# Optimization experiments

Measured on AMD Instinct MI355X. Metric: run time of the kernel, lower is better.

The kernel has to match this reference:

```python
import jax, jax.numpy as jnp
import numpy as np

N_NODES = 100000
N_EDGES = 1600000
IN_DIM, HID_DIM, OUT_DIM = 256, 128, 128


def gcn_norm(edge_index, edge_weight, num_nodes):
    # Add self-loops with weight 1 (PyG GCNConv default fill_value=1.0)
    loop = jnp.arange(num_nodes, dtype=edge_index.dtype)
    src = jnp.concatenate([edge_index[0], loop])
    dst = jnp.concatenate([edge_index[1], loop])
    w = jnp.concatenate([edge_weight, jnp.ones((num_nodes,), edge_weight.dtype)])
    # Symmetric normalization: deg computed at destination over edge weights
    deg = jax.ops.segment_sum(w, dst, num_segments=num_nodes)
    dinv = jnp.where(deg > 0, jax.lax.rsqrt(deg), 0.0)
    norm = dinv[src] * w * dinv[dst]  # [E + N]
    return src, dst, norm


def gcn_conv(x, W, b, src, dst, norm, num_nodes):
    h = x @ W                                  # [N, out]
    msg = h[src] * norm[:, None]               # gather + scale, [E+N, out]
    out = jax.ops.segment_sum(msg, dst, num_segments=num_nodes)  # scatter-add
    return out + b


def setup_inputs() -> dict:
    key = jax.random.key(0)
    ks = jax.random.split(key, 8)
    x = jax.random.normal(ks[0], (N_NODES, IN_DIM), dtype=jnp.float32)
    edge_index = jax.random.randint(ks[1], (2, N_EDGES), 0, N_NODES, dtype=jnp.int64)
    edge_weight = jax.random.uniform(ks[2], (N_EDGES,), dtype=jnp.float32)
    s1 = 1.0 / np.sqrt(IN_DIM)
    s2 = 1.0 / np.sqrt(HID_DIM)
    W1 = jax.random.uniform(ks[3], (IN_DIM, HID_DIM), jnp.float32, -s1, s1)
    b1 = jnp.zeros((HID_DIM,), jnp.float32)
    W2 = jax.random.uniform(ks[4], (HID_DIM, OUT_DIM), jnp.float32, -s2, s2)
    b2 = jnp.zeros((OUT_DIM,), jnp.float32)
    return {"x": x, "edge_index": edge_index, "edge_weight": edge_weight,
            "W1": W1, "b1": b1, "W2": W2, "b2": b2}


def reference(x, edge_index, edge_weight, W1, b1, W2, b2):
    n = x.shape[0]
    src, dst, norm = gcn_norm(edge_index, edge_weight, n)
    h = jax.nn.relu(gcn_conv(x, W1, b1, src, dst, norm, n))
    out = gcn_conv(h, W2, b2, src, dst, norm, n)
    return out
```

## Files before the change

kernel.cpp:

```cpp
#include <hip/hip_runtime.h>
#include <stdint.h>

#define N_NODES 100000
#define N_EDGES 1600000
#define IN_DIM 256
#define HID_DIM 128
#define OUT_DIM 128

#define NBUCK 391
#define CHUNK 4096

typedef __attribute__((ext_vector_type(8))) short short8;
typedef __attribute__((ext_vector_type(4))) float floatx4;

__device__ __forceinline__ float bf2f(unsigned short u) {
    union { unsigned int i; float f; } v; v.i = ((unsigned int)u) << 16; return v.f;
}
__device__ __forceinline__ unsigned short f2bf(float f) {
    union { float fl; unsigned int i; } v; v.fl = f;
    unsigned int x = v.i;
    return (unsigned short)((x + 0x7fffu + ((x >> 16) & 1u)) >> 16);
}
__device__ __forceinline__ float bflo(unsigned int u) {
    union { unsigned int i; float f; } v; v.i = u << 16; return v.f;
}
__device__ __forceinline__ float bfhi(unsigned int u) {
    union { unsigned int i; float f; } v; v.i = u & 0xffff0000u; return v.f;
}
__device__ __forceinline__ float asf(unsigned int u) {
    union { unsigned int i; float f; } v; v.i = u; return v.f;
}
__device__ __forceinline__ unsigned int asu(float f) {
    union { float fl; unsigned int i; } v; v.fl = f; return v.i;
}
__device__ __forceinline__ unsigned int pack2(float a, float b) {
    unsigned int ua = asu(a), ub = asu(b);
    ua += 0x7fffu + ((ua >> 16) & 1u);
    ub += 0x7fffu + ((ub >> 16) & 1u);
    return (ua >> 16) | (ub & 0xffff0000u);
}
__device__ __forceinline__ short8 pack8(float4 a, float4 b) {
    union { unsigned int u[4]; short8 s; } r;
    r.u[0] = pack2(a.x, a.y);
    r.u[1] = pack2(a.z, a.w);
    r.u[2] = pack2(b.x, b.y);
    r.u[3] = pack2(b.z, b.w);
    return r.s;
}

__global__ void k_detect(const unsigned int* __restrict__ xu, const unsigned int* __restrict__ eu,
                         int* __restrict__ flags, int* __restrict__ bucket_cnt) {
    __shared__ int s_huge, s_odd;
    if (threadIdx.x == 0) { s_huge = 0; s_odd = 0; }
    if (threadIdx.x < NBUCK) bucket_cnt[threadIdx.x] = 0;
    __syncthreads();
    int huge = 0, odd = 0;
    for (int i = threadIdx.x; i < 1024; i += 512) {
        unsigned int b = xu[i];
        unsigned int e = (b >> 23) & 0xffu;
        if (e >= 0xf0u) huge = 1;
        if (eu[2 * i + 1] != 0) odd = 1;
    }
    if (huge) atomicOr(&s_huge, 1);
    if (odd) atomicOr(&s_odd, 1);
    __syncthreads();
    if (threadIdx.x == 0) { flags[0] = s_huge ? 0 : 1; flags[1] = s_odd ? 0 : 1; }
}

__device__ __forceinline__ int load_idx(const void* base, long long i, int i64m) {
    int v = i64m ? (int)((const long long*)base)[i] : ((const int*)base)[i];
    return v < 0 ? 0 : (v >= N_NODES ? N_NODES - 1 : v);
}
__device__ __forceinline__ float load_f(const void* base, long long i, int f32m) {
    return f32m ? ((const float*)base)[i] : bf2f(((const unsigned short*)base)[i]);
}

__global__ void k_bhist(const void* __restrict__ ei, const int* __restrict__ flags,
                        int* __restrict__ bucket_cnt, int e) {
    __shared__ int h[NBUCK];
    for (int t = threadIdx.x; t < NBUCK; t += 256) h[t] = 0;
    __syncthreads();
    int i64m = flags[1];
    int base = blockIdx.x * CHUNK;
    int end = base + CHUNK < e ? base + CHUNK : e;
    for (int i = base + threadIdx.x; i < end; i += 256) {
        int d = load_idx(ei, (long long)N_EDGES + i, i64m);
        atomicAdd(&h[d >> 8], 1);
    }
    __syncthreads();
    for (int t = threadIdx.x; t < NBUCK; t += 256)
        if (h[t]) atomicAdd(&bucket_cnt[t], h[t]);
}

__global__ void k_bscan(const int* __restrict__ bucket_cnt, int* __restrict__ bucket_base,
                        int* __restrict__ bucket_cursor, int* __restrict__ rowptr) {
    __shared__ int lds[512];
    int t = threadIdx.x;
    int v = (t < NBUCK) ? bucket_cnt[t] : 0;
    lds[t] = v;
    __syncthreads();
    for (int off = 1; off < 512; off <<= 1) {
        int x = (t >= off) ? lds[t - off] : 0;
        __syncthreads();
        lds[t] += x;
        __syncthreads();
    }
    int excl = lds[t] - v;
    if (t < NBUCK) { bucket_base[t] = excl; bucket_cursor[t] = excl; }
    if (t == 0) { bucket_base[NBUCK] = lds[NBUCK - 1]; rowptr[N_NODES] = N_EDGES; }
}

__global__ void k_bscatter(const void* __restrict__ ei, const void* __restrict__ ew,
                           const int* __restrict__ flags, int* __restrict__ bucket_cursor,
                           uint2* __restrict__ ebuf, int e) {
    __shared__ int h[NBUCK];
    for (int t = threadIdx.x; t < NBUCK; t += 256) h[t] = 0;
    __syncthreads();
    int f32m = flags[0], i64m = flags[1];
    int base = blockIdx.x * CHUNK;
    int end = base + CHUNK < e ? base + CHUNK : e;
    for (int i = base + threadIdx.x; i < end; i += 256) {
        int d = load_idx(ei, (long long)N_EDGES + i, i64m);
        atomicAdd(&h[d >> 8], 1);
    }
    __syncthreads();
    for (int t = threadIdx.x; t < NBUCK; t += 256) {
        int c = h[t];
        h[t] = c ? atomicAdd(&bucket_cursor[t], c) : 0;
    }
    __syncthreads();
    for (int i = base + threadIdx.x; i < end; i += 256) {
        int s = load_idx(ei, i, i64m);
        int d = load_idx(ei, (long long)N_EDGES + i, i64m);
        float w = load_f(ew, i, f32m);
        int b = d >> 8;
        int p = atomicAdd(&h[b], 1);
        uint2 c; c.x = (unsigned int)s | ((unsigned int)(d & 255) << 17); c.y = asu(w);
        ebuf[p] = c;
    }
}

__global__ void k_fine(const uint2* __restrict__ ebuf, const int* __restrict__ bucket_base,
                       uint2* __restrict__ csr, int* __restrict__ rowptr,
                       float* __restrict__ dinv, int n) {
    __shared__ int h[256];
    __shared__ float fw[256];
    __shared__ int c2[256];
    int t = threadIdx.x, b = blockIdx.x;
    int e0 = bucket_base[b], e1 = bucket_base[b + 1];
    h[t] = 0; fw[t] = 0.f;
    __syncthreads();
    for (int i = e0 + t; i < e1; i += 256) {
        uint2 c = ebuf[i];
        int dl = (c.x >> 17) & 255;
        atomicAdd(&h[dl], 1);
        atomicAdd(&fw[dl], asf(c.y));
    }
    __syncthreads();
    int own = h[t];
    for (int off = 1; off < 256; off <<= 1) {
        int x = (t >= off) ? h[t - off] : 0;
        __syncthreads();
        h[t] += x;
        __syncthreads();
    }
    int excl = h[t] - own;
    int node = (b << 8) + t;
    if (node < n) {
        rowptr[node] = e0 + excl;
        dinv[node] = rsqrtf(1.0f + fw[t]);
    }
    c2[t] = e0 + excl;
    __syncthreads();
    for (int i = e0 + t; i < e1; i += 256) {
        uint2 c = ebuf[i];
        int dl = (c.x >> 17) & 255;
        int p = atomicAdd(&c2[dl], 1);
        csr[p] = c;
    }
}

__global__ void k_transpose(const void* __restrict__ W1, const void* __restrict__ W2,
                            const int* __restrict__ flags,
                            unsigned short* __restrict__ W1T, unsigned short* __restrict__ W2T) {
    int i = blockIdx.x * 256 + threadIdx.x;
    int f32m = flags[0];
    if (i < IN_DIM * HID_DIM) {
        int k = i / HID_DIM, n = i % HID_DIM;
        W1T[n * IN_DIM + k] = f2bf(load_f(W1, i, f32m));
    } else {
        int j = i - IN_DIM * HID_DIM;
        if (j < HID_DIM * OUT_DIM) {
            int k = j / OUT_DIM, n = j % OUT_DIM;
            W2T[n * HID_DIM + k] = f2bf(load_f(W2, j, f32m));
        }
    }
}

template <int K, bool F32M>
__device__ __forceinline__ void gemm_loop(const void* __restrict__ A,
                                          const unsigned short* __restrict__ Bs,
                                          size_t aoff0, size_t aoff1,
                                          int quad, int l16, floatx4 (&acc)[2][8]) {
    constexpr int NCH = K / 32;
    constexpr int BMASK = K / 8 - 1;
    float4 fraw[2][2];
    short8 braw[2];
    if (F32M) {
        const float* ap = (const float*)A;
        fraw[0][0] = *(const float4*)(ap + aoff0);
        fraw[0][1] = *(const float4*)(ap + aoff0 + 4);
        fraw[1][0] = *(const float4*)(ap + aoff1);
        fraw[1][1] = *(const float4*)(ap + aoff1 + 4);
    } else {
        const unsigned short* ap = (const unsigned short*)A;
        braw[0] = *(const short8*)(ap + aoff0);
        braw[1] = *(const short8*)(ap + aoff1);
    }
#pragma unroll
    for (int ch = 0; ch < NCH; ch++) {
        float4 nf[2][2];
        short8 nb[2];
        if (ch + 1 < NCH) {
            int o = (ch + 1) * 32;
            if (F32M) {
                const float* ap = (const float*)A;
                nf[0][0] = *(const float4*)(ap + aoff0 + o);
                nf[0][1] = *(const float4*)(ap + aoff0 + o + 4);
                nf[1][0] = *(const float4*)(ap + aoff1 + o);
                nf[1][1] = *(const float4*)(ap + aoff1 + o + 4);
            } else {
                const unsigned short* ap = (const unsigned short*)A;
                nb[0] = *(const short8*)(ap + aoff0 + o);
                nb[1] = *(const short8*)(ap + aoff1 + o);
            }
        }
        short8 a0, a1;
        if (F32M) {
            a0 = pack8(fraw[0][0], fraw[0][1]);
            a1 = pack8(fraw[1][0], fraw[1][1]);
        } else {
            a0 = braw[0];
            a1 = braw[1];
        }
#pragma unroll
        for (int c = 0; c < 8; c++) {
            int col = c * 16 + l16;
            int boff = col * K + 8 * ((ch * 4 + quad + (col & 7)) & BMASK);
            short8 bf = *(const short8*)(Bs + boff);
            acc[0][c] = __builtin_amdgcn_mfma_f32_16x16x32_bf16(a0, bf, acc[0][c], 0, 0, 0);
            acc[1][c] = __builtin_amdgcn_mfma_f32_16x16x32_bf16(a1, bf, acc[1][c], 0, 0, 0);
        }
        if (ch + 1 < NCH) {
            if (F32M) {
                fraw[0][0] = nf[0][0]; fraw[0][1] = nf[0][1];
                fraw[1][0] = nf[1][0]; fraw[1][1] = nf[1][1];
            } else {
                braw[0] = nb[0]; braw[1] = nb[1];
            }
        }
    }
}

template <int K, bool RAWA>
__global__ void k_gemm(const void* __restrict__ A, const unsigned short* __restrict__ WT,
                       unsigned short* __restrict__ H, const int* __restrict__ flags, int n) {
    __shared__ unsigned short Bs[128 * K];
    for (int base = threadIdx.x * 8; base < 128 * K; base += 256 * 8) {
        int col = base / K;
        int k = base - col * K;
        int ks = (k + (col & 7) * 8) & (K - 1);
        *(short8*)(&Bs[col * K + ks]) = *(const short8*)(WT + base);
    }
    __syncthreads();

    int wave = threadIdx.x >> 6;
    int lane = threadIdx.x & 63;
    int quad = lane >> 4;
    int l16 = lane & 15;
    int rowbase = blockIdx.x * 128 + wave * 32;
    int r0 = rowbase + l16;        if (r0 >= n) r0 = n - 1;
    int r1 = rowbase + 16 + l16;   if (r1 >= n) r1 = n - 1;
    size_t aoff0 = (size_t)r0 * K + quad * 8;
    size_t aoff1 = (size_t)r1 * K + quad * 8;

    floatx4 acc[2][8];
#pragma unroll
    for (int t = 0; t < 2; t++)
#pragma unroll
        for (int c = 0; c < 8; c++) acc[t][c] = (floatx4){0.f, 0.f, 0.f, 0.f};

    int f32m = RAWA ? flags[0] : 0;
    if (RAWA && f32m)
        gemm_loop<K, true>(A, Bs, aoff0, aoff1, quad, l16, acc);
    else
        gemm_loop<K, false>(A, Bs, aoff0, aoff1, quad, l16, acc);

#pragma unroll
    for (int t = 0; t < 2; t++)
#pragma unroll
        for (int c = 0; c < 8; c++)
#pragma unroll
            for (int r = 0; r < 4; r++) {
                int grow = rowbase + t * 16 + quad * 4 + r;
                if (grow < n) H[(size_t)grow * 128 + c * 16 + l16] = f2bf(acc[t][c][r]);
            }
}

template <bool RELU, bool FINAL>
__global__ void k_aggregate(const unsigned short* __restrict__ H, const int* __restrict__ rowptr,
                            const uint2* __restrict__ csr, const float* __restrict__ dinv,
                            const void* __restrict__ bias, void* __restrict__ out,
                            const int* __restrict__ flags, int n) {
    int node = blockIdx.x * 16 + (threadIdx.x >> 4);
    int lane = threadIdx.x & 15;
    if (node >= n) return;
    int col = lane * 8;
    int f32m = flags[0];

    float a0 = 0.f, a1 = 0.f, a2 = 0.f, a3 = 0.f;
    float a4 = 0.f, a5 = 0.f, a6 = 0.f, a7 = 0.f;
    int e0 = rowptr[node], e1 = rowptr[node + 1];
    int e = e0;
    for (; e + 4 <= e1; e += 4) {
        uint2 c0 = csr[e], c1 = csr[e + 1], c2 = csr[e + 2], c3 = csr[e + 3];
        int s0 = c0.x & 0x1FFFF, s1 = c1.x & 0x1FFFF, s2 = c2.x & 0x1FFFF, s3 = c3.x & 0x1FFFF;
        uint4 h0 = *(const uint4*)(H + (size_t)s0 * 128 + col);
        uint4 h1 = *(const uint4*)(H + (size_t)s1 * 128 + col);
        uint4 h2 = *(const uint4*)(H + (size_t)s2 * 128 + col);
        uint4 h3 = *(const uint4*)(H + (size_t)s3 * 128 + col);
        float w0 = asf(c0.y) * dinv[s0], w1 = asf(c1.y) * dinv[s1];
        float w2 = asf(c2.y) * dinv[s2], w3 = asf(c3.y) * dinv[s3];
        a0 += w0 * bflo(h0.x); a1 += w0 * bfhi(h0.x); a2 += w0 * bflo(h0.y); a3 += w0 * bfhi(h0.y);
        a4 += w0 * bflo(h0.z); a5 += w0 * bfhi(h0.z); a6 += w0 * bflo(h0.w); a7 += w0 * bfhi(h0.w);
        a0 += w1 * bflo(h1.x); a1 += w1 * bfhi(h1.x); a2 += w1 * bflo(h1.y); a3 += w1 * bfhi(h1.y);
        a4 += w1 * bflo(h1.z); a5 += w1 * bfhi(h1.z); a6 += w1 * bflo(h1.w); a7 += w1 * bfhi(h1.w);
        a0 += w2 * bflo(h2.x); a1 += w2 * bfhi(h2.x); a2 += w2 * bflo(h2.y); a3 += w2 * bfhi(h2.y);
        a4 += w2 * bflo(h2.z); a5 += w2 * bfhi(h2.z); a6 += w2 * bflo(h2.w); a7 += w2 * bfhi(h2.w);
        a0 += w3 * bflo(h3.x); a1 += w3 * bfhi(h3.x); a2 += w3 * bflo(h3.y); a3 += w3 * bfhi(h3.y);
        a4 += w3 * bflo(h3.z); a5 += w3 * bfhi(h3.z); a6 += w3 * bflo(h3.w); a7 += w3 * bfhi(h3.w);
    }
    for (; e < e1; e++) {
        uint2 c0 = csr[e];
        int s0 = c0.x & 0x1FFFF;
        uint4 h0 = *(const uint4*)(H + (size_t)s0 * 128 + col);
        float w0 = asf(c0.y) * dinv[s0];
        a0 += w0 * bflo(h0.x); a1 += w0 * bfhi(h0.x); a2 += w0 * bflo(h0.y); a3 += w0 * bfhi(h0.y);
        a4 += w0 * bflo(h0.z); a5 += w0 * bfhi(h0.z); a6 += w0 * bflo(h0.w); a7 += w0 * bfhi(h0.w);
    }

    float dn = dinv[node];
    float coef = dn * dn;
    uint4 u = *(const uint4*)(H + (size_t)node * 128 + col);
    a0 = dn * a0 + coef * bflo(u.x) + load_f(bias, col, f32m);
    a1 = dn * a1 + coef * bfhi(u.x) + load_f(bias, col + 1, f32m);
    a2 = dn * a2 + coef * bflo(u.y) + load_f(bias, col + 2, f32m);
    a3 = dn * a3 + coef * bfhi(u.y) + load_f(bias, col + 3, f32m);
    a4 = dn * a4 + coef * bflo(u.z) + load_f(bias, col + 4, f32m);
    a5 = dn * a5 + coef * bfhi(u.z) + load_f(bias, col + 5, f32m);
    a6 = dn * a6 + coef * bflo(u.w) + load_f(bias, col + 6, f32m);
    a7 = dn * a7 + coef * bfhi(u.w) + load_f(bias, col + 7, f32m);

    if (RELU) {
        a0 = fmaxf(a0, 0.f); a1 = fmaxf(a1, 0.f); a2 = fmaxf(a2, 0.f); a3 = fmaxf(a3, 0.f);
        a4 = fmaxf(a4, 0.f); a5 = fmaxf(a5, 0.f); a6 = fmaxf(a6, 0.f); a7 = fmaxf(a7, 0.f);
    }
    if (FINAL && f32m) {
        float* op = (float*)out + (size_t)node * 128 + col;
        float4 o0 = {a0, a1, a2, a3};
        float4 o1 = {a4, a5, a6, a7};
        *(float4*)op = o0;
        *(float4*)(op + 4) = o1;
    } else {
        uint4 o;
        o.x = pack2(a0, a1); o.y = pack2(a2, a3);
        o.z = pack2(a4, a5); o.w = pack2(a6, a7);
        *(uint4*)((unsigned short*)out + (size_t)node * 128 + col) = o;
    }
}

extern "C" void kernel_launch(void* const* d_in, const int* in_sizes, int n_in,
                              void* d_out, int out_size, void* d_ws, size_t ws_size,
                              hipStream_t stream) {
    const void* x  = d_in[0];
    const void* ei = d_in[1];
    const void* ew = d_in[2];
    const void* W1 = d_in[3];
    const void* b1 = d_in[4];
    const void* W2 = d_in[5];
    const void* b2 = d_in[6];

    char* p = (char*)d_ws;
    auto alloc = [&](size_t bytes) { char* r = p; p += (bytes + 255) & ~(size_t)255; return r; };
    int*   flags    = (int*)alloc(256);
    float* dinv     = (float*)alloc((size_t)N_NODES * 4);
    int*   rowptr   = (int*)alloc((size_t)(N_NODES + 1) * 4);
    int*   bucket_cnt    = (int*)alloc((size_t)NBUCK * 4);
    int*   bucket_base   = (int*)alloc((size_t)(NBUCK + 1) * 4);
    int*   bucket_cursor = (int*)alloc((size_t)NBUCK * 4);
    uint2* csr      = (uint2*)alloc((size_t)N_EDGES * 8);
    unsigned short* W1T  = (unsigned short*)alloc((size_t)IN_DIM * HID_DIM * 2);
    unsigned short* W2T  = (unsigned short*)alloc((size_t)HID_DIM * OUT_DIM * 2);
    unsigned short* hbuf = (unsigned short*)alloc((size_t)N_NODES * 128 * 2);
    unsigned short* zbuf = (unsigned short*)alloc((size_t)N_NODES * 128 * 2);
    uint2* ebuf = (uint2*)hbuf;

    int nbC = (N_EDGES + CHUNK - 1) / CHUNK;
    int nbG = (N_NODES + 127) / 128;
    int nbA = (N_NODES + 15) / 16;

    k_detect<<<1, 512, 0, stream>>>((const unsigned int*)x, (const unsigned int*)ei, flags, bucket_cnt);
    k_bhist<<<nbC, 256, 0, stream>>>(ei, flags, bucket_cnt, N_EDGES);
    k_bscan<<<1, 512, 0, stream>>>(bucket_cnt, bucket_base, bucket_cursor, rowptr);
    k_bscatter<<<nbC, 256, 0, stream>>>(ei, ew, flags, bucket_cursor, ebuf, N_EDGES);
    k_fine<<<NBUCK, 256, 0, stream>>>(ebuf, bucket_base, csr, rowptr, dinv, N_NODES);
    k_transpose<<<(IN_DIM * HID_DIM + HID_DIM * OUT_DIM + 255) / 256, 256, 0, stream>>>(W1, W2, flags, W1T, W2T);

    k_gemm<IN_DIM, true><<<nbG, 256, 0, stream>>>(x, W1T, hbuf, flags, N_NODES);
    k_aggregate<true, false><<<nbA, 256, 0, stream>>>(hbuf, rowptr, csr, dinv,
                                                      b1, zbuf, flags, N_NODES);
    k_gemm<HID_DIM, false><<<nbG, 256, 0, stream>>>(zbuf, W2T, hbuf, flags, N_NODES);
    k_aggregate<false, true><<<nbA, 256, 0, stream>>>(hbuf, rowptr, csr, dinv,
                                                      b2, d_out, flags, N_NODES);
}
```

Before: 431.5 us.

## Fold source dinv into CSR weights, split GEMM K staging, pipeline aggregate gathers

The weighted degree is now accumulated with global float atomics during the bucket scatter, and a small kernel turns it into dinv. The fine CSR pass can then premultiply each edge weight by dinv[src], which removes a random dinv gather per edge from both aggregation passes. The first-layer GEMM now stages W in two 128-wide K halves, halving its LDS footprint so more blocks can be resident, at the cost of an extra barrier and reload. The aggregate loop is software-pipelined to prefetch the next group of four neighbour rows while accumulating the current one. The trade-offs are 1.6M global atomics, one extra launch, and more registers in the aggregate kernel.

```diff
diff --git a/kernel.cpp b/kernel.cpp
--- a/kernel.cpp
+++ b/kernel.cpp
@@ -76,9 +76,11 @@
 }
 
 __global__ void k_bhist(const void* __restrict__ ei, const int* __restrict__ flags,
-                        int* __restrict__ bucket_cnt, int e) {
+                        int* __restrict__ bucket_cnt, float* __restrict__ wdeg, int e) {
     __shared__ int h[NBUCK];
     for (int t = threadIdx.x; t < NBUCK; t += 256) h[t] = 0;
+    int z = blockIdx.x * 256 + threadIdx.x;
+    if (z < N_NODES) wdeg[z] = 0.f;
     __syncthreads();
     int i64m = flags[1];
     int base = blockIdx.x * CHUNK;
@@ -112,7 +114,7 @@
 
 __global__ void k_bscatter(const void* __restrict__ ei, const void* __restrict__ ew,
                            const int* __restrict__ flags, int* __restrict__ bucket_cursor,
-                           uint2* __restrict__ ebuf, int e) {
+                           uint2* __restrict__ ebuf, float* __restrict__ wdeg, int e) {
     __shared__ int h[NBUCK];
     for (int t = threadIdx.x; t < NBUCK; t += 256) h[t] = 0;
     __syncthreads();
@@ -133,6 +135,7 @@
         int s = load_idx(ei, i, i64m);
         int d = load_idx(ei, (long long)N_EDGES + i, i64m);
         float w = load_f(ew, i, f32m);
+        atomicAdd(&wdeg[d], w);
         int b = d >> 8;
         int p = atomicAdd(&h[b], 1);
         uint2 c; c.x = (unsigned int)s | ((unsigned int)(d & 255) << 17); c.y = asu(w);
@@ -140,21 +143,24 @@
     }
 }
 
+__global__ void k_dinv(const float* __restrict__ wdeg, float* __restrict__ dinv, int n) {
+    int i = blockIdx.x * 256 + threadIdx.x;
+    if (i < n) dinv[i] = rsqrtf(1.0f + wdeg[i]);
+}
+
 __global__ void k_fine(const uint2* __restrict__ ebuf, const int* __restrict__ bucket_base,
-                       uint2* __restrict__ csr, int* __restrict__ rowptr,
-                       float* __restrict__ dinv, int n) {
+                       const float* __restrict__ dinv, uint2* __restrict__ csr,
+                       int* __restrict__ rowptr, int n) {
     __shared__ int h[256];
-    __shared__ float fw[256];
     __shared__ int c2[256];
     int t = threadIdx.x, b = blockIdx.x;
     int e0 = bucket_base[b], e1 = bucket_base[b + 1];
-    h[t] = 0; fw[t] = 0.f;
+    h[t] = 0;
     __syncthreads();
     for (int i = e0 + t; i < e1; i += 256) {
         uint2 c = ebuf[i];
         int dl = (c.x >> 17) & 255;
         atomicAdd(&h[dl], 1);
-        atomicAdd(&fw[dl], asf(c.y));
     }
     __syncthreads();
     int own = h[t];
@@ -166,16 +172,14 @@
     }
     int excl = h[t] - own;
     int node = (b << 8) + t;
-    if (node < n) {
-        rowptr[node] = e0 + excl;
-        dinv[node] = rsqrtf(1.0f + fw[t]);
-    }
+    if (node < n) rowptr[node] = e0 + excl;
     c2[t] = e0 + excl;
     __syncthreads();
     for (int i = e0 + t; i < e1; i += 256) {
         uint2 c = ebuf[i];
         int dl = (c.x >> 17) & 255;
         int p = atomicAdd(&c2[dl], 1);
+        c.y = asu(asf(c.y) * dinv[c.x & 0x1FFFF]);
         csr[p] = c;
     }
 }
@@ -197,13 +201,13 @@
     }
 }
 
-template <int K, bool F32M>
+template <int KH, bool F32M>
 __device__ __forceinline__ void gemm_loop(const void* __restrict__ A,
                                           const unsigned short* __restrict__ Bs,
                                           size_t aoff0, size_t aoff1,
                                           int quad, int l16, floatx4 (&acc)[2][8]) {
-    constexpr int NCH = K / 32;
-    constexpr int BMASK = K / 8 - 1;
+    constexpr int NCH = KH / 32;
+    constexpr int BMASK = KH / 8 - 1;
     float4 fraw[2][2];
     short8 braw[2];
     if (F32M) {
@@ -246,7 +250,7 @@
 #pragma unroll
         for (int c = 0; c < 8; c++) {
             int col = c * 16 + l16;
-            int boff = col * K + 8 * ((ch * 4 + quad + (col & 7)) & BMASK);
+            int boff = col * KH + 8 * ((ch * 4 + quad + (col & 7)) & BMASK);
             short8 bf = *(const short8*)(Bs + boff);
             acc[0][c] = __builtin_amdgcn_mfma_f32_16x16x32_bf16(a0, bf, acc[0][c], 0, 0, 0);
             acc[1][c] = __builtin_amdgcn_mfma_f32_16x16x32_bf16(a1, bf, acc[1][c], 0, 0, 0);
@@ -265,14 +269,8 @@
 template <int K, bool RAWA>
 __global__ void k_gemm(const void* __restrict__ A, const unsigned short* __restrict__ WT,
                        unsigned short* __restrict__ H, const int* __restrict__ flags, int n) {
-    __shared__ unsigned short Bs[128 * K];
-    for (int base = threadIdx.x * 8; base < 128 * K; base += 256 * 8) {
-        int col = base / K;
-        int k = base - col * K;
-        int ks = (k + (col & 7) * 8) & (K - 1);
-        *(short8*)(&Bs[col * K + ks]) = *(const short8*)(WT + base);
-    }
-    __syncthreads();
+    constexpr int KH = (K > 128) ? 128 : K;
+    __shared__ unsigned short Bs[128 * KH];
 
     int wave = threadIdx.x >> 6;
     int lane = threadIdx.x & 63;
@@ -291,10 +289,22 @@
         for (int c = 0; c < 8; c++) acc[t][c] = (floatx4){0.f, 0.f, 0.f, 0.f};
 
     int f32m = RAWA ? flags[0] : 0;
-    if (RAWA && f32m)
-        gemm_loop<K, true>(A, Bs, aoff0, aoff1, quad, l16, acc);
-    else
-        gemm_loop<K, false>(A, Bs, aoff0, aoff1, quad, l16, acc);
+
+#pragma unroll
+    for (int hh = 0; hh < K / KH; hh++) {
+        if (hh) __syncthreads();
+        for (int base = threadIdx.x * 8; base < 128 * KH; base += 256 * 8) {
+            int col = base / KH;
+            int k = base - col * KH;
+            int ks = (k + (col & 7) * 8) & (KH - 1);
+            *(short8*)(&Bs[col * KH + ks]) = *(const short8*)(WT + col * K + hh * KH + k);
+        }
+        __syncthreads();
+        if (RAWA && f32m)
+            gemm_loop<KH, true>(A, Bs, aoff0 + hh * KH, aoff1 + hh * KH, quad, l16, acc);
+        else
+            gemm_loop<KH, false>(A, Bs, aoff0 + hh * KH, aoff1 + hh * KH, quad, l16, acc);
+    }
 
 #pragma unroll
     for (int t = 0; t < 2; t++)
@@ -305,6 +315,13 @@
                 int grow = rowbase + t * 16 + quad * 4 + r;
                 if (grow < n) H[(size_t)grow * 128 + c * 16 + l16] = f2bf(acc[t][c][r]);
             }
+}
+
+__device__ __forceinline__ void acc8(float wt, uint4 hv, float* a) {
+    a[0] += wt * bflo(hv.x); a[1] += wt * bfhi(hv.x);
+    a[2] += wt * bflo(hv.y); a[3] += wt * bfhi(hv.y);
+    a[4] += wt * bflo(hv.z); a[5] += wt * bfhi(hv.z);
+    a[6] += wt * bflo(hv.w); a[7] += wt * bfhi(hv.w);
 }
 
 template <bool RELU, bool FINAL>
@@ -318,63 +335,69 @@
     int col = lane * 8;
     int f32m = flags[0];
 
-    float a0 = 0.f, a1 = 0.f, a2 = 0.f, a3 = 0.f;
-    float a4 = 0.f, a5 = 0.f, a6 = 0.f, a7 = 0.f;
     int e0 = rowptr[node], e1 = rowptr[node + 1];
-    int e = e0;
-    for (; e + 4 <= e1; e += 4) {
-        uint2 c0 = csr[e], c1 = csr[e + 1], c2 = csr[e + 2], c3 = csr[e + 3];
-        int s0 = c0.x & 0x1FFFF, s1 = c1.x & 0x1FFFF, s2 = c2.x & 0x1FFFF, s3 = c3.x & 0x1FFFF;
-        uint4 h0 = *(const uint4*)(H + (size_t)s0 * 128 + col);
-        uint4 h1 = *(const uint4*)(H + (size_t)s1 * 128 + col);
-        uint4 h2 = *(const uint4*)(H + (size_t)s2 * 128 + col);
-        uint4 h3 = *(const uint4*)(H + (size_t)s3 * 128 + col);
-        float w0 = asf(c0.y) * dinv[s0], w1 = asf(c1.y) * dinv[s1];
-        float w2 = asf(c2.y) * dinv[s2], w3 = asf(c3.y) * dinv[s3];
-        a0 += w0 * bflo(h0.x); a1 += w0 * bfhi(h0.x); a2 += w0 * bflo(h0.y); a3 += w0 * bfhi(h0.y);
-        a4 += w0 * bflo(h0.z); a5 += w0 * bfhi(h0.z); a6 += w0 * bflo(h0.w); a7 += w0 * bfhi(h0.w);
-        a0 += w1 * bflo(h1.x); a1 += w1 * bfhi(h1.x); a2 += w1 * bflo(h1.y); a3 += w1 * bfhi(h1.y);
-        a4 += w1 * bflo(h1.z); a5 += w1 * bfhi(h1.z); a6 += w1 * bflo(h1.w); a7 += w1 * bfhi(h1.w);
-        a0 += w2 * bflo(h2.x); a1 += w2 * bfhi(h2.x); a2 += w2 * bflo(h2.y); a3 += w2 * bfhi(h2.y);
-        a4 += w2 * bflo(h2.z); a5 += w2 * bfhi(h2.z); a6 += w2 * bflo(h2.w); a7 += w2 * bfhi(h2.w);
-        a0 += w3 * bflo(h3.x); a1 += w3 * bfhi(h3.x); a2 += w3 * bflo(h3.y); a3 += w3 * bfhi(h3.y);
-        a4 += w3 * bflo(h3.z); a5 += w3 * bfhi(h3.z); a6 += w3 * bflo(h3.w); a7 += w3 * bfhi(h3.w);
-    }
-    for (; e < e1; e++) {
-        uint2 c0 = csr[e];
-        int s0 = c0.x & 0x1FFFF;
-        uint4 h0 = *(const uint4*)(H + (size_t)s0 * 128 + col);
-        float w0 = asf(c0.y) * dinv[s0];
-        a0 += w0 * bflo(h0.x); a1 += w0 * bfhi(h0.x); a2 += w0 * bflo(h0.y); a3 += w0 * bfhi(h0.y);
-        a4 += w0 * bflo(h0.z); a5 += w0 * bfhi(h0.z); a6 += w0 * bflo(h0.w); a7 += w0 * bfhi(h0.w);
-    }
-
+    uint4 u = *(const uint4*)(H + (size_t)node * 128 + col);
     float dn = dinv[node];
+
+    float a[8] = {0.f, 0.f, 0.f, 0.f, 0.f, 0.f, 0.f, 0.f};
+
+    const uint2* ep = csr + e0;
+    int nb = (e1 - e0) >> 2;
+    uint2 c0, c1, c2, c3;
+    uint4 h0, h1, h2, h3;
+    if (nb) {
+        c0 = ep[0]; c1 = ep[1]; c2 = ep[2]; c3 = ep[3];
+        h0 = *(const uint4*)(H + (size_t)(c0.x & 0x1FFFF) * 128 + col);
+        h1 = *(const uint4*)(H + (size_t)(c1.x & 0x1FFFF) * 128 + col);
+        h2 = *(const uint4*)(H + (size_t)(c2.x & 0x1FFFF) * 128 + col);
+        h3 = *(const uint4*)(H + (size_t)(c3.x & 0x1FFFF) * 128 + col);
+    }
+    for (int b = 1; b < nb; b++) {
+        const uint2* np = ep + 4 * b;
+        uint2 d0 = np[0], d1 = np[1], d2 = np[2], d3 = np[3];
+        uint4 g0 = *(const uint4*)(H + (size_t)(d0.x & 0x1FFFF) * 128 + col);
+        uint4 g1 = *(const uint4*)(H + (size_t)(d1.x & 0x1FFFF) * 128 + col);
+        uint4 g2 = *(const uint4*)(H + (size_t)(d2.x & 0x1FFFF) * 128 + col);
+        uint4 g3 = *(const uint4*)(H + (size_t)(d3.x & 0x1FFFF) * 128 + col);
+        acc8(asf(c0.y), h0, a); acc8(asf(c1.y), h1, a);
+        acc8(asf(c2.y), h2, a); acc8(asf(c3.y), h3, a);
+        c0 = d0; c1 = d1; c2 = d2; c3 = d3;
+        h0 = g0; h1 = g1; h2 = g2; h3 = g3;
+    }
+    if (nb) {
+        acc8(asf(c0.y), h0, a); acc8(asf(c1.y), h1, a);
+        acc8(asf(c2.y), h2, a); acc8(asf(c3.y), h3, a);
+    }
+    for (int e = e0 + (nb << 2); e < e1; e++) {
+        uint2 c = csr[e];
+        uint4 hh = *(const uint4*)(H + (size_t)(c.x & 0x1FFFF) * 128 + col);
+        acc8(asf(c.y), hh, a);
+    }
+
     float coef = dn * dn;
-    uint4 u = *(const uint4*)(H + (size_t)node * 128 + col);
-    a0 = dn * a0 + coef * bflo(u.x) + load_f(bias, col, f32m);
-    a1 = dn * a1 + coef * bfhi(u.x) + load_f(bias, col + 1, f32m);
-    a2 = dn * a2 + coef * bflo(u.y) + load_f(bias, col + 2, f32m);
-    a3 = dn * a3 + coef * bfhi(u.y) + load_f(bias, col + 3, f32m);
-    a4 = dn * a4 + coef * bflo(u.z) + load_f(bias, col + 4, f32m);
-    a5 = dn * a5 + coef * bfhi(u.z) + load_f(bias, col + 5, f32m);
-    a6 = dn * a6 + coef * bflo(u.w) + load_f(bias, col + 6, f32m);
-    a7 = dn * a7 + coef * bfhi(u.w) + load_f(bias, col + 7, f32m);
+    a[0] = dn * a[0] + coef * bflo(u.x) + load_f(bias, col, f32m);
+    a[1] = dn * a[1] + coef * bfhi(u.x) + load_f(bias, col + 1, f32m);
+    a[2] = dn * a[2] + coef * bflo(u.y) + load_f(bias, col + 2, f32m);
+    a[3] = dn * a[3] + coef * bfhi(u.y) + load_f(bias, col + 3, f32m);
+    a[4] = dn * a[4] + coef * bflo(u.z) + load_f(bias, col + 4, f32m);
+    a[5] = dn * a[5] + coef * bfhi(u.z) + load_f(bias, col + 5, f32m);
+    a[6] = dn * a[6] + coef * bflo(u.w) + load_f(bias, col + 6, f32m);
+    a[7] = dn * a[7] + coef * bfhi(u.w) + load_f(bias, col + 7, f32m);
 
     if (RELU) {
-        a0 = fmaxf(a0, 0.f); a1 = fmaxf(a1, 0.f); a2 = fmaxf(a2, 0.f); a3 = fmaxf(a3, 0.f);
-        a4 = fmaxf(a4, 0.f); a5 = fmaxf(a5, 0.f); a6 = fmaxf(a6, 0.f); a7 = fmaxf(a7, 0.f);
+#pragma unroll
+        for (int i = 0; i < 8; i++) a[i] = fmaxf(a[i], 0.f);
     }
     if (FINAL && f32m) {
         float* op = (float*)out + (size_t)node * 128 + col;
-        float4 o0 = {a0, a1, a2, a3};
-        float4 o1 = {a4, a5, a6, a7};
+        float4 o0 = {a[0], a[1], a[2], a[3]};
+        float4 o1 = {a[4], a[5], a[6], a[7]};
         *(float4*)op = o0;
         *(float4*)(op + 4) = o1;
     } else {
         uint4 o;
-        o.x = pack2(a0, a1); o.y = pack2(a2, a3);
-        o.z = pack2(a4, a5); o.w = pack2(a6, a7);
+        o.x = pack2(a[0], a[1]); o.y = pack2(a[2], a[3]);
+        o.z = pack2(a[4], a[5]); o.w = pack2(a[6], a[7]);
         *(uint4*)((unsigned short*)out + (size_t)node * 128 + col) = o;
     }
 }
@@ -394,6 +417,7 @@
     auto alloc = [&](size_t bytes) { char* r = p; p += (bytes + 255) & ~(size_t)255; return r; };
     int*   flags    = (int*)alloc(256);
     float* dinv     = (float*)alloc((size_t)N_NODES * 4);
+    float* wdeg     = (float*)alloc((size_t)N_NODES * 4);
     int*   rowptr   = (int*)alloc((size_t)(N_NODES + 1) * 4);
     int*   bucket_cnt    = (int*)alloc((size_t)NBUCK * 4);
     int*   bucket_base   = (int*)alloc((size_t)(NBUCK + 1) * 4);
@@ -406,14 +430,16 @@
     uint2* ebuf = (uint2*)hbuf;
 
     int nbC = (N_EDGES + CHUNK - 1) / CHUNK;
+    int nbN = (N_NODES + 255) / 256;
     int nbG = (N_NODES + 127) / 128;
     int nbA = (N_NODES + 15) / 16;
 
     k_detect<<<1, 512, 0, stream>>>((const unsigned int*)x, (const unsigned int*)ei, flags, bucket_cnt);
-    k_bhist<<<nbC, 256, 0, stream>>>(ei, flags, bucket_cnt, N_EDGES);
+    k_bhist<<<nbC, 256, 0, stream>>>(ei, flags, bucket_cnt, wdeg, N_EDGES);
     k_bscan<<<1, 512, 0, stream>>>(bucket_cnt, bucket_base, bucket_cursor, rowptr);
-    k_bscatter<<<nbC, 256, 0, stream>>>(ei, ew, flags, bucket_cursor, ebuf, N_EDGES);
-    k_fine<<<NBUCK, 256, 0, stream>>>(ebuf, bucket_base, csr, rowptr, dinv, N_NODES);
+    k_bscatter<<<nbC, 256, 0, stream>>>(ei, ew, flags, bucket_cursor, ebuf, wdeg, N_EDGES);
+    k_dinv<<<nbN, 256, 0, stream>>>(wdeg, dinv, N_NODES);
+    k_fine<<<NBUCK, 256, 0, stream>>>(ebuf, bucket_base, dinv, csr, rowptr, N_NODES);
     k_transpose<<<(IN_DIM * HID_DIM + HID_DIM * OUT_DIM + 255) / 256, 256, 0, stream>>>(W1, W2, flags, W1T, W2T);
 
     k_gemm<IN_DIM, true><<<nbG, 256, 0, stream>>>(x, W1T, hbuf, flags, N_NODES);
```

Result: slower. 513.0 us (+18.9%).
